# Kernel tuning notes

Measured on AMD Instinct MI355X. Metric: run time of the kernel, lower is better.

## Reference

```python
import jax, jax.numpy as jnp
import numpy as np
import math

B, S, D_MODEL, N_HEAD = 4, 2048, 1024, 16
D_K = D_MODEL // N_HEAD
ROPE_THETA = 10000.0


def _rope(x):
    # x: [B, H, S, Dk]; interleaved-pair rotary embedding.
    b, h, s, d = x.shape
    inv_freq = ROPE_THETA ** (-jnp.arange(0, d, 2, dtype=jnp.float32) / d)  # [d/2]
    ang = jnp.arange(s, dtype=jnp.float32)[:, None] * inv_freq[None, :]      # [S, d/2]
    cos, sin = jnp.cos(ang), jnp.sin(ang)
    x1, x2 = x[..., 0::2], x[..., 1::2]
    r1 = x1 * cos - x2 * sin
    r2 = x1 * sin + x2 * cos
    return jnp.stack([r1, r2], axis=-1).reshape(b, h, s, d)


def setup_inputs() -> dict:
    key = jax.random.key(0)
    ks = jax.random.split(key, 7)
    sc = 1.0 / math.sqrt(D_MODEL)
    return {
        "q": jax.random.normal(ks[0], (B, S, D_MODEL), jnp.float32),
        "k": jax.random.normal(ks[1], (B, S, D_MODEL), jnp.float32),
        "v": jax.random.normal(ks[2], (B, S, D_MODEL), jnp.float32),
        "Wq": jax.random.normal(ks[3], (D_MODEL, D_MODEL), jnp.float32) * sc,
        "Wk": jax.random.normal(ks[4], (D_MODEL, D_MODEL), jnp.float32) * sc,
        "Wv": jax.random.normal(ks[5], (D_MODEL, D_MODEL), jnp.float32) * sc,
        "Wo": jax.random.normal(ks[6], (D_MODEL, D_MODEL), jnp.float32) * sc,
    }


def _split(x):
    b, s, d = x.shape
    return x.reshape(b, s, N_HEAD, d // N_HEAD).transpose(0, 2, 1, 3)  # [B,H,S,Dk]


def reference(q, k, v, Wq, Wk, Wv, Wo):
    q = jnp.einsum("bsd,de->bse", q, Wq)
    k = jnp.einsum("bsd,de->bse", k, Wk)
    v = jnp.einsum("bsd,de->bse", v, Wv)
    qh, kh, vh = _split(q), _split(k), _split(v)
    qh, kh = _rope(qh), _rope(kh)
    scale = 1.0 / math.sqrt(D_K)
    score = jnp.einsum("bhqd,bhkd->bhqk", qh, kh) * scale  # [B,H,S,S]
    attn = jax.nn.softmax(score, axis=-1)
    out = jnp.einsum("bhqk,bhkd->bhqd", attn, vh)
    out = out.transpose(0, 2, 1, 3).reshape(q.shape[0], q.shape[1], D_MODEL)
    return jnp.einsum("bsd,de->bse", out, Wo)
```

## Files before the change

### kernel.cpp

```cpp
#include <hip/hip_runtime.h>
#include <stdint.h>

#define Bv 4
#define Sv 2048
#define Dv 1024
#define Hv 16
#define DKv 64
#define BSv (Bv * Sv)

typedef unsigned short u16;
typedef __attribute__((ext_vector_type(8))) short short8;
typedef __attribute__((ext_vector_type(8))) unsigned short u16x8;
typedef __attribute__((ext_vector_type(4))) unsigned short u16x4;
typedef __attribute__((ext_vector_type(4))) float f32x4;
typedef __attribute__((ext_vector_type(16))) float f32x16;

__device__ __forceinline__ u16 f2bf(float f) {
  union { float f; uint32_t u; } x; x.f = f;
  uint32_t r = x.u + 0x7FFFu + ((x.u >> 16) & 1u);
  return (u16)(r >> 16);
}

__device__ __forceinline__ uint32_t cvtpk(float lo, float hi) {
  uint32_t r;
  asm("v_cvt_pk_bf16_f32 %0, %1, %2" : "=v"(r) : "v"(lo), "v"(hi));
  return r;
}

__device__ __forceinline__ void gl_lds16(const void* g, void* l) {
  __builtin_amdgcn_global_load_lds(
      (__attribute__((address_space(1))) void*)g,
      (__attribute__((address_space(3))) void*)l, 16, 0, 0);
}

__device__ __forceinline__ f32x4 mfma16(short8 a, short8 b, f32x4 c) {
  return __builtin_amdgcn_mfma_f32_16x16x32_bf16(a, b, c, 0, 0, 0);
}
__device__ __forceinline__ f32x16 mfma32(short8 a, short8 b, f32x16 c) {
  return __builtin_amdgcn_mfma_f32_32x32x16_bf16(a, b, c, 0, 0, 0);
}

template <int N>
__device__ __forceinline__ void vwait() {
  asm volatile("s_waitcnt vmcnt(%0)" ::"n"(N) : "memory");
}
__device__ __forceinline__ void bar() {
  asm volatile("" ::: "memory");
  __builtin_amdgcn_s_barrier();
  asm volatile("" ::: "memory");
}
template <int N>
__device__ __forceinline__ void tsync() {
  asm volatile("s_waitcnt vmcnt(%0) lgkmcnt(0)" ::"n"(N) : "memory");
  __builtin_amdgcn_s_barrier();
  __builtin_amdgcn_sched_barrier(0);
}

__global__ __launch_bounds__(256) void conv_wt(
    const float* __restrict__ w0, const float* __restrict__ w1,
    const float* __restrict__ w2, const float* __restrict__ w3,
    u16* __restrict__ t0, u16* __restrict__ t1, u16* __restrict__ t2,
    u16* __restrict__ t3) {
  const float* W = (blockIdx.z == 0) ? w0 : (blockIdx.z == 1 ? w1 : (blockIdx.z == 2 ? w2 : w3));
  u16* T = (blockIdx.z == 0) ? t0 : (blockIdx.z == 1 ? t1 : (blockIdx.z == 2 ? t2 : t3));
  __shared__ u16 tile[64][72];
  int nb = blockIdx.x * 64, kb = blockIdx.y * 64;
  int t = threadIdx.x;
#pragma unroll
  for (int p = 0; p < 4; ++p) {
    int idx = p * 256 + t;
    int r = idx >> 4;
    int c4 = (idx & 15) * 4;
    float4 vv = *(const float4*)(W + (size_t)(kb + r) * Dv + nb + c4);
    tile[c4 + 0][r] = f2bf(vv.x);
    tile[c4 + 1][r] = f2bf(vv.y);
    tile[c4 + 2][r] = f2bf(vv.z);
    tile[c4 + 3][r] = f2bf(vv.w);
  }
  __syncthreads();
#pragma unroll
  for (int p = 0; p < 4; ++p) {
    int idx = p * 256 + t;
    int r = idx >> 4;
    int c4 = (idx & 15) * 4;
    u16x4 o = { tile[r][c4], tile[r][c4 + 1], tile[r][c4 + 2], tile[r][c4 + 3] };
    *(u16x4*)(T + (size_t)(nb + r) * Dv + kb + c4) = o;
  }
}

__global__ __launch_bounds__(256, 2) void gemm_qkv(
    const float* __restrict__ A0, const float* __restrict__ A1, const float* __restrict__ A2,
    const u16* __restrict__ B0, const u16* __restrict__ B1, const u16* __restrict__ B2,
    u16* __restrict__ O0, u16* __restrict__ O1, u16* __restrict__ O2) {
  __shared__ u16 As[2][128 * 64];
  __shared__ u16 Bs[2][128 * 64];
  int z = blockIdx.z;
  const float* A = (z == 0) ? A0 : (z == 1 ? A1 : A2);
  const u16* Bt  = (z == 0) ? B0 : (z == 1 ? B1 : B2);
  u16* Out       = (z == 0) ? O0 : (z == 1 ? O1 : O2);
  int mode = z;

  int tid = threadIdx.x;
  int lane = tid & 63, wid = tid >> 6;
  int quad = lane >> 4, cc = lane & 15;
  int wm = (wid >> 1) * 64, wn = (wid & 1) * 64;
  int m0 = blockIdx.x * 128, n0 = blockIdx.y * 128;

  f32x4 acc[4][4];
#pragma unroll
  for (int mi = 0; mi < 4; ++mi)
#pragma unroll
    for (int ni = 0; ni < 4; ++ni) {
      f32x4 zf = {0.f, 0.f, 0.f, 0.f};
      acc[mi][ni] = zf;
    }

  auto stageB = [&](int ki, int b) {
#pragma unroll
    for (int p = 0; p < 4; ++p) {
      int slot = p * 256 + tid;
      int row = slot >> 3, cl = slot & 7;
      int cg = cl ^ (row & 7);
      gl_lds16(Bt + (size_t)(n0 + row) * Dv + ki * 64 + cg * 8, &Bs[b][slot * 8]);
    }
  };

  float4 fa0[4][2], fa1[4][2];
  auto loadA = [&](int ki, float4 (&fs)[4][2]) {
#pragma unroll
    for (int p = 0; p < 4; ++p) {
      int slot = p * 256 + tid;
      int row = slot >> 3, cl = slot & 7;
      int cg = cl ^ (row & 7);
      const float* g = A + (size_t)(m0 + row) * Dv + ki * 64 + cg * 8;
      fs[p][0] = *(const float4*)g;
      fs[p][1] = *(const float4*)(g + 4);
    }
  };
  auto writeA = [&](int b, const float4 (&fs)[4][2]) {
#pragma unroll
    for (int p = 0; p < 4; ++p) {
      int slot = p * 256 + tid;
      union { uint32_t u[4]; u16x8 s; } o;
      o.u[0] = cvtpk(fs[p][0].x, fs[p][0].y);
      o.u[1] = cvtpk(fs[p][0].z, fs[p][0].w);
      o.u[2] = cvtpk(fs[p][1].x, fs[p][1].y);
      o.u[3] = cvtpk(fs[p][1].z, fs[p][1].w);
      *(u16x8*)&As[b][slot * 8] = o.s;
    }
  };
  auto computeTile = [&](int cur) {
#pragma unroll
    for (int kk = 0; kk < 2; ++kk) {
      short8 af[4], bfr[4];
#pragma unroll
      for (int mi = 0; mi < 4; ++mi) {
        int row = wm + mi * 16 + cc;
        int cg = kk * 4 + quad;
        af[mi] = *(const short8*)&As[cur][row * 64 + (cg ^ (row & 7)) * 8];
      }
#pragma unroll
      for (int ni = 0; ni < 4; ++ni) {
        int row = wn + ni * 16 + cc;
        int cg = kk * 4 + quad;
        bfr[ni] = *(const short8*)&Bs[cur][row * 64 + (cg ^ (row & 7)) * 8];
      }
#pragma unroll
      for (int mi = 0; mi < 4; ++mi)
#pragma unroll
        for (int ni = 0; ni < 4; ++ni)
          acc[mi][ni] = mfma16(af[mi], bfr[ni], acc[mi][ni]);
    }
  };

  loadA(0, fa0); writeA(0, fa0); stageB(0, 0);
  asm volatile("" ::: "memory");
  loadA(1, fa1);

  const int NT = Dv / 64;
#pragma unroll 1
  for (int tt = 0; tt < NT; tt += 2) {
    tsync<8>();
    if (tt + 1 < NT) stageB(tt + 1, 1);
    asm volatile("" ::: "memory");
    if (tt + 2 < NT) loadA(tt + 2, fa0);
    computeTile(0);
    if (tt + 1 < NT) writeA(1, fa1);
    if (tt + 2 < NT) tsync<8>(); else tsync<0>();
    if (tt + 2 < NT) stageB(tt + 2, 0);
    asm volatile("" ::: "memory");
    if (tt + 3 < NT) loadA(tt + 3, fa1);
    computeTile(1);
    if (tt + 2 < NT) writeA(0, fa0);
  }

  if (mode <= 1) {
    float postscale = (mode == 0) ? 0.18033688011112042f : 1.0f;
#pragma unroll
    for (int ni = 0; ni < 4; ++ni) {
      int n = n0 + wn + ni * 16 + cc;
      int h = n >> 6, d = n & 63;
      float inv = __expf(-(float)(d & 62) * (9.210340372f / 64.0f));
      float sign = (d & 1) ? 1.0f : -1.0f;
#pragma unroll
      for (int mi = 0; mi < 4; ++mi) {
        int mB = m0 + wm + mi * 16 + quad * 4;
#pragma unroll
        for (int r = 0; r < 4; ++r) {
          int m = mB + r;
          int b = m >> 11, s = m & (Sv - 1);
          float val = acc[mi][ni][r];
          float part = __shfl_xor(val, 1);
          float sn, cs;
          __sincosf((float)s * inv, &sn, &cs);
          float outv = (val * cs + sign * part * sn) * postscale;
          Out[((size_t)(b * Hv + h) * Sv + s) * DKv + d] = f2bf(outv);
        }
      }
    }
  } else {
#pragma unroll
    for (int ni = 0; ni < 4; ++ni) {
      int n = n0 + wn + ni * 16 + cc;
      int h = n >> 6, d = n & 63;
#pragma unroll
      for (int mi = 0; mi < 4; ++mi) {
        int mB = m0 + wm + mi * 16 + quad * 4;
        int b = mB >> 11, s = mB & (Sv - 1);
        u16x4 o4 = { f2bf(acc[mi][ni][0]), f2bf(acc[mi][ni][1]),
                     f2bf(acc[mi][ni][2]), f2bf(acc[mi][ni][3]) };
        *(u16x4*)&Out[((size_t)(b * Hv + h) * DKv + d) * Sv + s] = o4;
      }
    }
  }
}

__global__ __launch_bounds__(512, 2) void gemm_bt(
    const u16* __restrict__ A0, const u16* __restrict__ A1, const u16* __restrict__ A2,
    const u16* __restrict__ B0, const u16* __restrict__ B1, const u16* __restrict__ B2,
    void* __restrict__ O0, void* __restrict__ O1, void* __restrict__ O2,
    int modeSel) {
  __shared__ u16 As[3][256 * 64];
  __shared__ u16 Bs[3][128 * 64];
  int z = blockIdx.z;
  const u16* A  = (z == 0) ? A0 : (z == 1 ? A1 : A2);
  const u16* Bt = (z == 0) ? B0 : (z == 1 ? B1 : B2);
  void* Out     = (z == 0) ? O0 : (z == 1 ? O1 : O2);
  int mode = (modeSel < 0) ? z : modeSel;

  int tid = threadIdx.x;
  int lane = tid & 63, wid = tid >> 6;
  int quad = lane >> 4, cc = lane & 15;
  int wm = (wid >> 1) * 64, wn = (wid & 1) * 64;
  int bx = blockIdx.x;
  int swz = (bx & 7) * 32 + (bx >> 3);
  int m0 = (swz >> 3) * 256, n0 = (swz & 7) * 128;

  f32x4 acc[4][4];
#pragma unroll
  for (int mi = 0; mi < 4; ++mi)
#pragma unroll
    for (int ni = 0; ni < 4; ++ni) {
      f32x4 zf = {0.f, 0.f, 0.f, 0.f};
      acc[mi][ni] = zf;
    }

  auto stageA2 = [&](int ki, int b, int p0) {
#pragma unroll
    for (int p = 0; p < 2; ++p) {
      int slot = (p0 + p) * 512 + tid;
      int row = slot >> 3, cl = slot & 7;
      int cg = cl ^ (row & 7);
      gl_lds16(A + (size_t)(m0 + row) * Dv + ki * 64 + cg * 8, &As[b][slot * 8]);
    }
  };
  auto stageB1 = [&](int ki, int b, int p0) {
    int slot = p0 * 512 + tid;
    int row = slot >> 3, cl = slot & 7;
    int cg = cl ^ (row & 7);
    gl_lds16(Bt + (size_t)(n0 + row) * Dv + ki * 64 + cg * 8, &Bs[b][slot * 8]);
  };

  stageA2(0, 0, 0); stageA2(0, 0, 2); stageB1(0, 0, 0); stageB1(0, 0, 1);
  stageA2(1, 1, 0); stageA2(1, 1, 2); stageB1(1, 1, 0); stageB1(1, 1, 1);
  vwait<6>();
  bar();

  const int NT = Dv / 64;
  int cur = 0, nxt = 2;
#pragma unroll 1
  for (int t = 0; t < NT; ++t) {
    const u16* Ac = &As[cur][0];
    const u16* Bc = &Bs[cur][0];
#pragma unroll
    for (int kk = 0; kk < 2; ++kk) {
      short8 af[4], bfr[4];
#pragma unroll
      for (int mi = 0; mi < 4; ++mi) {
        int row = wm + mi * 16 + cc;
        int cg = kk * 4 + quad;
        af[mi] = *(const short8*)&Ac[row * 64 + (cg ^ (row & 7)) * 8];
      }
#pragma unroll
      for (int ni = 0; ni < 4; ++ni) {
        int row = wn + ni * 16 + cc;
        int cg = kk * 4 + quad;
        bfr[ni] = *(const short8*)&Bc[row * 64 + (cg ^ (row & 7)) * 8];
      }
      if (t + 2 < NT) {
        if (kk == 0) { stageA2(t + 2, nxt, 0); stageB1(t + 2, nxt, 0); }
        else         { stageA2(t + 2, nxt, 2); stageB1(t + 2, nxt, 1); }
      }
      bar();
      __builtin_amdgcn_s_setprio(1);
#pragma unroll
      for (int mi = 0; mi < 4; ++mi)
#pragma unroll
        for (int ni = 0; ni < 4; ++ni)
          acc[mi][ni] = mfma16(af[mi], bfr[ni], acc[mi][ni]);
      __builtin_amdgcn_s_setprio(0);
      if (kk == 0) bar();
    }
    if (t < NT - 1) {
      if (t + 2 < NT) vwait<6>(); else vwait<0>();
      bar();
    }
    cur = (cur == 2) ? 0 : cur + 1;
    nxt = (nxt == 2) ? 0 : nxt + 1;
  }

  if (mode <= 1) {
    u16* O = (u16*)Out;
    float postscale = (mode == 0) ? 0.18033688011112042f : 1.0f;
#pragma unroll
    for (int ni = 0; ni < 4; ++ni) {
      int n = n0 + wn + ni * 16 + cc;
      int h = n >> 6, d = n & 63;
      float inv = __expf(-(float)(d & 62) * (9.210340372f / 64.0f));
      float sign = (d & 1) ? 1.0f : -1.0f;
#pragma unroll
      for (int mi = 0; mi < 4; ++mi) {
        int mB = m0 + wm + mi * 16 + quad * 4;
#pragma unroll
        for (int r = 0; r < 4; ++r) {
          int m = mB + r;
          int b = m >> 11, s = m & (Sv - 1);
          float val = acc[mi][ni][r];
          float part = __shfl_xor(val, 1);
          float sn, cs;
          __sincosf((float)s * inv, &sn, &cs);
          float outv = (val * cs + sign * part * sn) * postscale;
          O[((size_t)(b * Hv + h) * Sv + s) * DKv + d] = f2bf(outv);
        }
      }
    }
  } else if (mode == 2) {
    u16* O = (u16*)Out;
#pragma unroll
    for (int ni = 0; ni < 4; ++ni) {
      int n = n0 + wn + ni * 16 + cc;
      int h = n >> 6, d = n & 63;
#pragma unroll
      for (int mi = 0; mi < 4; ++mi) {
        int mB = m0 + wm + mi * 16 + quad * 4;
        int b = mB >> 11, s = mB & (Sv - 1);
        u16x4 o4 = { f2bf(acc[mi][ni][0]), f2bf(acc[mi][ni][1]),
                     f2bf(acc[mi][ni][2]), f2bf(acc[mi][ni][3]) };
        *(u16x4*)&O[((size_t)(b * Hv + h) * DKv + d) * Sv + s] = o4;
      }
    }
  } else {
    float* O = (float*)Out;
#pragma unroll
    for (int ni = 0; ni < 4; ++ni) {
      int n = n0 + wn + ni * 16 + cc;
#pragma unroll
      for (int mi = 0; mi < 4; ++mi) {
        int mB = m0 + wm + mi * 16 + quad * 4;
#pragma unroll
        for (int r = 0; r < 4; ++r)
          O[(size_t)(mB + r) * Dv + n] = acc[mi][ni][r];
      }
    }
  }
}

__global__ __launch_bounds__(256, 2) void attn(
    const u16* __restrict__ Qp, const u16* __restrict__ Kp,
    const u16* __restrict__ Vt, u16* __restrict__ ctx) {
  __shared__ u16 Ks[2][64 * 64];
  __shared__ u16 Vs[2][64 * 64];
  int tid = threadIdx.x;
  int lane = tid & 63, wid = tid >> 6;
  int hi = lane >> 5, c32 = lane & 31;
  int sz = (c32 & 7) ^ ((c32 >> 3) & 3);
  int bh = blockIdx.y;
  int q0 = blockIdx.x * 256 + wid * 64;
  const u16* Qh = Qp + (size_t)bh * Sv * DKv;
  const u16* Kh = Kp + (size_t)bh * Sv * DKv;
  const u16* Vh = Vt + (size_t)bh * Sv * DKv;

  const short8 ones = { (short)0x3F80, (short)0x3F80, (short)0x3F80, (short)0x3F80,
                        (short)0x3F80, (short)0x3F80, (short)0x3F80, (short)0x3F80 };

  short8 qf[2][4];
#pragma unroll
  for (int qs = 0; qs < 2; ++qs)
#pragma unroll
    for (int dk = 0; dk < 4; ++dk)
      qf[qs][dk] = *(const short8*)&Qh[(size_t)(q0 + qs * 32 + c32) * DKv + dk * 16 + hi * 8];

  f32x16 o[2][2];
  f32x16 ol[2];
#pragma unroll
  for (int qs = 0; qs < 2; ++qs) {
#pragma unroll
    for (int dt = 0; dt < 2; ++dt)
#pragma unroll
      for (int r = 0; r < 16; ++r) o[qs][dt][r] = 0.f;
#pragma unroll
    for (int r = 0; r < 16; ++r) ol[qs][r] = 0.f;
  }

#pragma unroll
  for (int p = 0; p < 2; ++p) {
    int slot = p * 256 + tid;
    int row = slot >> 3, cl = slot & 7;
    int cg = cl ^ ((row & 7) ^ ((row >> 3) & 3));
    gl_lds16(Kh + (size_t)row * DKv + cg * 8, &Ks[0][slot * 8]);
    gl_lds16(Vh + (size_t)row * Sv + cg * 8, &Vs[0][slot * 8]);
  }

  for (int kt = 0; kt < Sv / 64; ++kt) {
    int cur = kt & 1;
    __syncthreads();

    if (kt + 1 < Sv / 64) {
      int s1 = (kt + 1) * 64;
#pragma unroll
      for (int p = 0; p < 2; ++p) {
        int slot = p * 256 + tid;
        int row = slot >> 3, cl = slot & 7;
        int cg = cl ^ ((row & 7) ^ ((row >> 3) & 3));
        gl_lds16(Kh + (size_t)(s1 + row) * DKv + cg * 8, &Ks[1 - cur][slot * 8]);
        gl_lds16(Vh + (size_t)row * Sv + s1 + cg * 8, &Vs[1 - cur][slot * 8]);
      }
    }

#pragma unroll
    for (int half = 0; half < 2; ++half) {
      short8 kf[4];
#pragma unroll
      for (int dk = 0; dk < 4; ++dk)
        kf[dk] = *(const short8*)&Ks[cur][(half * 32 + c32) * 64 + (((dk * 2 + hi) ^ sz)) * 8];

      f32x16 st[2];
#pragma unroll
      for (int qs = 0; qs < 2; ++qs) {
#pragma unroll
        for (int r = 0; r < 16; ++r) st[qs][r] = 0.f;
#pragma unroll
        for (int dk = 0; dk < 4; ++dk)
          st[qs] = mfma32(kf[dk], qf[qs][dk], st[qs]);
      }

#pragma unroll
      for (int pp = 0; pp < 2; ++pp) {
        int pk = half * 2 + pp;
        short8 vf[2];
#pragma unroll
        for (int dt = 0; dt < 2; ++dt)
          vf[dt] = *(const short8*)&Vs[cur][(dt * 32 + c32) * 64 + (((pk * 2 + hi) ^ sz)) * 8];
#pragma unroll
        for (int qs = 0; qs < 2; ++qs) {
          float e0 = __builtin_amdgcn_exp2f(st[qs][8 * pp + 0]);
          float e1 = __builtin_amdgcn_exp2f(st[qs][8 * pp + 1]);
          float e2 = __builtin_amdgcn_exp2f(st[qs][8 * pp + 2]);
          float e3 = __builtin_amdgcn_exp2f(st[qs][8 * pp + 3]);
          float e4 = __builtin_amdgcn_exp2f(st[qs][8 * pp + 4]);
          float e5 = __builtin_amdgcn_exp2f(st[qs][8 * pp + 5]);
          float e6 = __builtin_amdgcn_exp2f(st[qs][8 * pp + 6]);
          float e7 = __builtin_amdgcn_exp2f(st[qs][8 * pp + 7]);
          uint32_t plo0 = __builtin_amdgcn_perm(__float_as_uint(e1), __float_as_uint(e0), 0x07060302u);
          uint32_t plo1 = __builtin_amdgcn_perm(__float_as_uint(e3), __float_as_uint(e2), 0x07060302u);
          uint32_t phi0 = __builtin_amdgcn_perm(__float_as_uint(e5), __float_as_uint(e4), 0x07060302u);
          uint32_t phi1 = __builtin_amdgcn_perm(__float_as_uint(e7), __float_as_uint(e6), 0x07060302u);
          uint32_t s0 = hi ? plo0 : phi0;
          uint32_t s1 = hi ? plo1 : phi1;
          uint32_t r0 = (uint32_t)__shfl_xor((int)s0, 32);
          uint32_t r1 = (uint32_t)__shfl_xor((int)s1, 32);
          union { uint32_t u[4]; short8 s8; } pu;
          pu.u[0] = hi ? r0 : plo0;
          pu.u[1] = hi ? r1 : plo1;
          pu.u[2] = hi ? phi0 : r0;
          pu.u[3] = hi ? phi1 : r1;
          ol[qs] = mfma32(pu.s8, ones, ol[qs]);
          o[qs][0] = mfma32(pu.s8, vf[0], o[qs][0]);
          o[qs][1] = mfma32(pu.s8, vf[1], o[qs][1]);
        }
      }
    }
  }

  int b = bh >> 4, h = bh & 15;
#pragma unroll
  for (int qs = 0; qs < 2; ++qs)
#pragma unroll
    for (int r = 0; r < 16; ++r) {
      int q = q0 + qs * 32 + (r & 3) + 8 * (r >> 2) + 4 * hi;
      float linv = 1.0f / ol[qs][r];
#pragma unroll
      for (int dt = 0; dt < 2; ++dt) {
        int d = h * DKv + dt * 32 + c32;
        ctx[((size_t)b * Sv + q) * Dv + d] = f2bf(o[qs][dt][r] * linv);
      }
    }
}

extern "C" void kernel_launch(void* const* d_in, const int* in_sizes, int n_in,
                              void* d_out, int out_size, void* d_ws, size_t ws_size,
                              hipStream_t stream) {
  (void)in_sizes; (void)n_in; (void)out_size; (void)ws_size;
  const float* q  = (const float*)d_in[0];
  const float* k  = (const float*)d_in[1];
  const float* v  = (const float*)d_in[2];
  const float* Wq = (const float*)d_in[3];
  const float* Wk = (const float*)d_in[4];
  const float* Wv = (const float*)d_in[5];
  const float* Wo = (const float*)d_in[6];

  char* ws = (char*)d_ws;
  size_t off = 0;
  const size_t big = (size_t)BSv * Dv * sizeof(u16);
  const size_t wsz = (size_t)Dv * Dv * sizeof(u16);
  u16* Wqt = (u16*)(ws + off); off += wsz;
  u16* Wkt = (u16*)(ws + off); off += wsz;
  u16* Wvt = (u16*)(ws + off); off += wsz;
  u16* Wot = (u16*)(ws + off); off += wsz;
  u16* Qp  = (u16*)(ws + off); off += big;
  u16* Kp  = (u16*)(ws + off); off += big;
  u16* Vtr = (u16*)(ws + off); off += big;
  u16* ctx = (u16*)(ws + off); off += big;

  conv_wt<<<dim3(Dv / 64, Dv / 64, 4), 256, 0, stream>>>(Wq, Wk, Wv, Wo, Wqt, Wkt, Wvt, Wot);
  gemm_qkv<<<dim3(BSv / 128, Dv / 128, 3), 256, 0, stream>>>(
      q, k, v, Wqt, Wkt, Wvt, Qp, Kp, Vtr);
  attn<<<dim3(Sv / 256, Bv * Hv), 256, 0, stream>>>(Qp, Kp, Vtr, ctx);
  gemm_bt<<<dim3(256, 1, 1), 512, 0, stream>>>(
      ctx, ctx, ctx, Wot, Wot, Wot, d_out, d_out, d_out, 3);
}
```

Baseline: 328.5 us.

## Replace triple-buffered 256x128 output GEMM with simpler double-buffered 128x128 kernel

Replaces the generic multi-mode gemm_bt output projection with a dedicated gemm_out kernel. It uses 128x128 tiles, 256 threads and two LDS buffers with a __syncthreads per k-step, in place of 256x128 tiles, 512 threads, three-stage buffering, setprio and block swizzling. The smaller tile doubles the grid to 512 blocks and lowers LDS use, which may allow better occupancy. In exchange it gives up the deeper prefetch, the L2-friendly swizzle and the larger per-block reuse. The loads are also not waited on explicitly before the barrier, so correctness depends on __syncthreads draining vmcnt.

```diff
diff --git a/kernel.cpp b/kernel.cpp
--- a/kernel.cpp
+++ b/kernel.cpp
@@ -40,15 +40,6 @@
   return __builtin_amdgcn_mfma_f32_32x32x16_bf16(a, b, c, 0, 0, 0);
 }
 
-template <int N>
-__device__ __forceinline__ void vwait() {
-  asm volatile("s_waitcnt vmcnt(%0)" ::"n"(N) : "memory");
-}
-__device__ __forceinline__ void bar() {
-  asm volatile("" ::: "memory");
-  __builtin_amdgcn_s_barrier();
-  asm volatile("" ::: "memory");
-}
 template <int N>
 __device__ __forceinline__ void tsync() {
   asm volatile("s_waitcnt vmcnt(%0) lgkmcnt(0)" ::"n"(N) : "memory");
@@ -235,26 +226,17 @@
   }
 }
 
-__global__ __launch_bounds__(512, 2) void gemm_bt(
-    const u16* __restrict__ A0, const u16* __restrict__ A1, const u16* __restrict__ A2,
-    const u16* __restrict__ B0, const u16* __restrict__ B1, const u16* __restrict__ B2,
-    void* __restrict__ O0, void* __restrict__ O1, void* __restrict__ O2,
-    int modeSel) {
-  __shared__ u16 As[3][256 * 64];
-  __shared__ u16 Bs[3][128 * 64];
-  int z = blockIdx.z;
-  const u16* A  = (z == 0) ? A0 : (z == 1 ? A1 : A2);
-  const u16* Bt = (z == 0) ? B0 : (z == 1 ? B1 : B2);
-  void* Out     = (z == 0) ? O0 : (z == 1 ? O1 : O2);
-  int mode = (modeSel < 0) ? z : modeSel;
+__global__ __launch_bounds__(256) void gemm_out(
+    const u16* __restrict__ A, const u16* __restrict__ Bt,
+    float* __restrict__ O) {
+  __shared__ u16 As[2][128 * 64];
+  __shared__ u16 Bs[2][128 * 64];
 
   int tid = threadIdx.x;
   int lane = tid & 63, wid = tid >> 6;
   int quad = lane >> 4, cc = lane & 15;
   int wm = (wid >> 1) * 64, wn = (wid & 1) * 64;
-  int bx = blockIdx.x;
-  int swz = (bx & 7) * 32 + (bx >> 3);
-  int m0 = (swz >> 3) * 256, n0 = (swz & 7) * 128;
+  int m0 = blockIdx.x * 128, n0 = blockIdx.y * 128;
 
   f32x4 acc[4][4];
 #pragma unroll
@@ -265,33 +247,31 @@
       acc[mi][ni] = zf;
     }
 
-  auto stageA2 = [&](int ki, int b, int p0) {
-#pragma unroll
-    for (int p = 0; p < 2; ++p) {
-      int slot = (p0 + p) * 512 + tid;
-      int row = slot >> 3, cl = slot & 7;
-      int cg = cl ^ (row & 7);
-      gl_lds16(A + (size_t)(m0 + row) * Dv + ki * 64 + cg * 8, &As[b][slot * 8]);
-    }
-  };
-  auto stageB1 = [&](int ki, int b, int p0) {
-    int slot = p0 * 512 + tid;
+#pragma unroll
+  for (int p = 0; p < 4; ++p) {
+    int slot = p * 256 + tid;
     int row = slot >> 3, cl = slot & 7;
     int cg = cl ^ (row & 7);
-    gl_lds16(Bt + (size_t)(n0 + row) * Dv + ki * 64 + cg * 8, &Bs[b][slot * 8]);
-  };
-
-  stageA2(0, 0, 0); stageA2(0, 0, 2); stageB1(0, 0, 0); stageB1(0, 0, 1);
-  stageA2(1, 1, 0); stageA2(1, 1, 2); stageB1(1, 1, 0); stageB1(1, 1, 1);
-  vwait<6>();
-  bar();
-
-  const int NT = Dv / 64;
-  int cur = 0, nxt = 2;
-#pragma unroll 1
-  for (int t = 0; t < NT; ++t) {
-    const u16* Ac = &As[cur][0];
-    const u16* Bc = &Bs[cur][0];
+    gl_lds16(A + (size_t)(m0 + row) * Dv + cg * 8, &As[0][slot * 8]);
+    gl_lds16(Bt + (size_t)(n0 + row) * Dv + cg * 8, &Bs[0][slot * 8]);
+  }
+
+  for (int ki = 0; ki < Dv / 64; ++ki) {
+    int cur = ki & 1;
+    __syncthreads();
+
+    if (ki + 1 < Dv / 64) {
+      int k1 = (ki + 1) * 64;
+#pragma unroll
+      for (int p = 0; p < 4; ++p) {
+        int slot = p * 256 + tid;
+        int row = slot >> 3, cl = slot & 7;
+        int cg = cl ^ (row & 7);
+        gl_lds16(A + (size_t)(m0 + row) * Dv + k1 + cg * 8, &As[1 - cur][slot * 8]);
+        gl_lds16(Bt + (size_t)(n0 + row) * Dv + k1 + cg * 8, &Bs[1 - cur][slot * 8]);
+      }
+    }
+
 #pragma unroll
     for (int kk = 0; kk < 2; ++kk) {
       short8 af[4], bfr[4];
@@ -299,88 +279,31 @@
       for (int mi = 0; mi < 4; ++mi) {
         int row = wm + mi * 16 + cc;
         int cg = kk * 4 + quad;
-        af[mi] = *(const short8*)&Ac[row * 64 + (cg ^ (row & 7)) * 8];
+        af[mi] = *(const short8*)&As[cur][row * 64 + (cg ^ (row & 7)) * 8];
       }
 #pragma unroll
       for (int ni = 0; ni < 4; ++ni) {
         int row = wn + ni * 16 + cc;
         int cg = kk * 4 + quad;
-        bfr[ni] = *(const short8*)&Bc[row * 64 + (cg ^ (row & 7)) * 8];
-      }
-      if (t + 2 < NT) {
-        if (kk == 0) { stageA2(t + 2, nxt, 0); stageB1(t + 2, nxt, 0); }
-        else         { stageA2(t + 2, nxt, 2); stageB1(t + 2, nxt, 1); }
-      }
-      bar();
-      __builtin_amdgcn_s_setprio(1);
+        bfr[ni] = *(const short8*)&Bs[cur][row * 64 + (cg ^ (row & 7)) * 8];
+      }
 #pragma unroll
       for (int mi = 0; mi < 4; ++mi)
 #pragma unroll
         for (int ni = 0; ni < 4; ++ni)
           acc[mi][ni] = mfma16(af[mi], bfr[ni], acc[mi][ni]);
-      __builtin_amdgcn_s_setprio(0);
-      if (kk == 0) bar();
-    }
-    if (t < NT - 1) {
-      if (t + 2 < NT) vwait<6>(); else vwait<0>();
-      bar();
-    }
-    cur = (cur == 2) ? 0 : cur + 1;
-    nxt = (nxt == 2) ? 0 : nxt + 1;
-  }
-
-  if (mode <= 1) {
-    u16* O = (u16*)Out;
-    float postscale = (mode == 0) ? 0.18033688011112042f : 1.0f;
-#pragma unroll
-    for (int ni = 0; ni < 4; ++ni) {
-      int n = n0 + wn + ni * 16 + cc;
-      int h = n >> 6, d = n & 63;
-      float inv = __expf(-(float)(d & 62) * (9.210340372f / 64.0f));
-      float sign = (d & 1) ? 1.0f : -1.0f;
-#pragma unroll
-      for (int mi = 0; mi < 4; ++mi) {
-        int mB = m0 + wm + mi * 16 + quad * 4;
-#pragma unroll
-        for (int r = 0; r < 4; ++r) {
-          int m = mB + r;
-          int b = m >> 11, s = m & (Sv - 1);
-          float val = acc[mi][ni][r];
-          float part = __shfl_xor(val, 1);
-          float sn, cs;
-          __sincosf((float)s * inv, &sn, &cs);
-          float outv = (val * cs + sign * part * sn) * postscale;
-          O[((size_t)(b * Hv + h) * Sv + s) * DKv + d] = f2bf(outv);
-        }
-      }
-    }
-  } else if (mode == 2) {
-    u16* O = (u16*)Out;
-#pragma unroll
-    for (int ni = 0; ni < 4; ++ni) {
-      int n = n0 + wn + ni * 16 + cc;
-      int h = n >> 6, d = n & 63;
-#pragma unroll
-      for (int mi = 0; mi < 4; ++mi) {
-        int mB = m0 + wm + mi * 16 + quad * 4;
-        int b = mB >> 11, s = mB & (Sv - 1);
-        u16x4 o4 = { f2bf(acc[mi][ni][0]), f2bf(acc[mi][ni][1]),
-                     f2bf(acc[mi][ni][2]), f2bf(acc[mi][ni][3]) };
-        *(u16x4*)&O[((size_t)(b * Hv + h) * DKv + d) * Sv + s] = o4;
-      }
-    }
-  } else {
-    float* O = (float*)Out;
-#pragma unroll
-    for (int ni = 0; ni < 4; ++ni) {
-      int n = n0 + wn + ni * 16 + cc;
-#pragma unroll
-      for (int mi = 0; mi < 4; ++mi) {
-        int mB = m0 + wm + mi * 16 + quad * 4;
-#pragma unroll
-        for (int r = 0; r < 4; ++r)
-          O[(size_t)(mB + r) * Dv + n] = acc[mi][ni][r];
-      }
+    }
+  }
+
+#pragma unroll
+  for (int ni = 0; ni < 4; ++ni) {
+    int n = n0 + wn + ni * 16 + cc;
+#pragma unroll
+    for (int mi = 0; mi < 4; ++mi) {
+      int mB = m0 + wm + mi * 16 + quad * 4;
+#pragma unroll
+      for (int r = 0; r < 4; ++r)
+        O[(size_t)(mB + r) * Dv + n] = acc[mi][ni][r];
     }
   }
 }
@@ -546,6 +469,5 @@
   gemm_qkv<<<dim3(BSv / 128, Dv / 128, 3), 256, 0, stream>>>(
       q, k, v, Wqt, Wkt, Wvt, Qp, Kp, Vtr);
   attn<<<dim3(Sv / 256, Bv * Hv), 256, 0, stream>>>(Qp, Kp, Vtr, ctx);
-  gemm_bt<<<dim3(256, 1, 1), 512, 0, stream>>>(
-      ctx, ctx, ctx, Wot, Wot, Wot, d_out, d_out, d_out, 3);
-}
+  gemm_out<<<dim3(BSv / 128, Dv / 128), 256, 0, stream>>>(ctx, Wot, (float*)d_out);
+}
```

Result: no change. 325.5 us (-0.9%).
